# Kernel optimization log

Hardware: AMD Instinct MI355X
Metric: run time of the kernel (lower is better)

Reference implementation:

```python
import jax, jax.numpy as jnp
import numpy as np

N_NODES = 50000
N_EDGES = 600000
EMB = 128

def setup_inputs() -> dict:
    key = jax.random.key(0)
    ks = jax.random.split(key, 6)
    h = jax.random.normal(ks[0], (N_NODES, EMB), dtype=jnp.float32)
    edge_attr = jax.random.normal(ks[1], (N_EDGES, EMB), dtype=jnp.float32)
    src = jax.random.randint(ks[2], (N_EDGES,), 0, N_NODES, dtype=jnp.int32)
    dst = jax.random.randint(ks[3], (N_EDGES,), 0, N_NODES, dtype=jnp.int32)
    # MLP: Linear(emb, 2*emb) -> ReLU -> Linear(2*emb, emb)
    W1 = jax.random.normal(ks[4], (EMB, 2 * EMB), dtype=jnp.float32) * (1.0 / np.sqrt(EMB))
    b1 = jnp.zeros((2 * EMB,), dtype=jnp.float32)
    W2 = jax.random.normal(ks[5], (2 * EMB, EMB), dtype=jnp.float32) * (1.0 / np.sqrt(2 * EMB))
    b2 = jnp.zeros((EMB,), dtype=jnp.float32)
    eps = jnp.zeros((1,), dtype=jnp.float32)
    return {"h": h, "edge_attr": edge_attr, "src": src, "dst": dst,
            "W1": W1, "b1": b1, "W2": W2, "b2": b2, "eps": eps}

def reference(h, edge_attr, src, dst, W1, b1, W2, b2, eps):
    # message: m_e = h[src_e] + edge_attr_e   (edge_encoder is None)
    m = h[src] + edge_attr                              # [E, D]
    # reduce: sum messages per destination node
    aggr = jax.ops.segment_sum(m, dst, num_segments=N_NODES)  # [N, D]
    # out = (1 + eps) * h + MLP(aggr)
    hidden = jax.nn.relu(aggr @ W1 + b1)                # [N, 2D]
    mlp_out = hidden @ W2 + b2                          # [N, D]
    return (1.0 + eps) * h + mlp_out
```

## Files before the change

kernel.cpp:

```cpp
#include <hip/hip_runtime.h>
#include <hip/hip_bf16.h>

#define N_NODES 50000
#define N_EDGES 600000
#define D 128
#define H2 256
#define TN 16
#define MAXC 2048

__global__ __launch_bounds__(256) void hist_kernel(const int* __restrict__ dst,
                                                   int* __restrict__ counts) {
    unsigned int e = blockIdx.x * 256u + threadIdx.x;
    if (e < N_EDGES) atomicAdd(&counts[dst[e]], 1);
}

__global__ __launch_bounds__(256) void scan1_kernel(const int* __restrict__ counts,
                                                    int* __restrict__ scanned,
                                                    int* __restrict__ blocksums) {
    __shared__ int wsum[4];
    const int tid = threadIdx.x;
    const int lane = tid & 63;
    const int wv = tid >> 6;
    const int i = blockIdx.x * 256 + tid;
    const int cval = (i < N_NODES) ? counts[i] : 0;
    int x = cval;
    #pragma unroll
    for (int d = 1; d < 64; d <<= 1) {
        int t = __shfl_up(x, d, 64);
        if (lane >= d) x += t;
    }
    if (lane == 63) wsum[wv] = x;
    __syncthreads();
    if (tid == 0) {
        int s = 0;
        #pragma unroll
        for (int w = 0; w < 4; ++w) { s += wsum[w]; wsum[w] = s; }
    }
    __syncthreads();
    const int prefix = (wv > 0 ? wsum[wv - 1] : 0) + (x - cval);
    if (i < N_NODES) scanned[i] = prefix;
    if (tid == 0) blocksums[blockIdx.x] = wsum[3];
}

__global__ __launch_bounds__(256) void scan2_kernel(const int* __restrict__ blocksums,
                                                    int* __restrict__ blockbase, int nb) {
    __shared__ int wsum[4];
    const int tid = threadIdx.x;
    const int lane = tid & 63;
    const int wv = tid >> 6;
    const int cval = (tid < nb) ? blocksums[tid] : 0;
    int x = cval;
    #pragma unroll
    for (int d = 1; d < 64; d <<= 1) {
        int t = __shfl_up(x, d, 64);
        if (lane >= d) x += t;
    }
    if (lane == 63) wsum[wv] = x;
    __syncthreads();
    if (tid == 0) {
        int s = 0;
        #pragma unroll
        for (int w = 0; w < 4; ++w) { s += wsum[w]; wsum[w] = s; }
    }
    __syncthreads();
    if (tid < nb) blockbase[tid] = (wv > 0 ? wsum[wv - 1] : 0) + (x - cval);
}

__global__ __launch_bounds__(256) void scan3_kernel(const int* __restrict__ scanned,
                                                    const int* __restrict__ blockbase,
                                                    int* __restrict__ offsets,
                                                    int* __restrict__ cursor) {
    const int i = blockIdx.x * 256 + threadIdx.x;
    if (i < N_NODES) {
        const int v = scanned[i] + blockbase[blockIdx.x];
        offsets[i] = v;
        cursor[i] = v;
    }
    if (i == 0) offsets[N_NODES] = N_EDGES;
}

__global__ __launch_bounds__(256) void scatter_kernel(const int* __restrict__ src,
                                                      const int* __restrict__ dst,
                                                      int* __restrict__ cursor,
                                                      int2* __restrict__ perm2) {
    unsigned int e = blockIdx.x * 256u + threadIdx.x;
    if (e >= N_EDGES) return;
    const int d = dst[e];
    const int p = atomicAdd(&cursor[d], 1);
    perm2[p] = make_int2((int)e | ((d & (TN - 1)) << 20), src[e]);
}

__global__ __launch_bounds__(256) void fused_kernel(
    const float* __restrict__ h, const float* __restrict__ ea,
    const int* __restrict__ offsets, const int2* __restrict__ perm2,
    const float* __restrict__ W1, const float* __restrict__ b1,
    const float* __restrict__ W2, const float* __restrict__ b2,
    const float* __restrict__ eps, float* __restrict__ out)
{
    __shared__ float s_aggr[TN][D];
    __shared__ float s_hidden[TN][H2];
    int2* s_perm = (int2*)&s_hidden[0][0];

    const int tid = threadIdx.x;
    const int node0 = blockIdx.x * TN;

    for (int i = tid; i < TN * D / 4; i += 256)
        ((float4*)s_aggr)[i] = make_float4(0.f, 0.f, 0.f, 0.f);

    const int beg = offsets[node0];
    const int end = offsets[node0 + TN];
    const int grp = tid >> 5;
    const int c = (tid & 31) << 2;

    for (int cb = beg; cb < end; cb += MAXC) {
        const int cnt = min(end - cb, MAXC);
        __syncthreads();
        for (int i = tid; i < cnt; i += 256) s_perm[i] = perm2[cb + i];
        __syncthreads();
        const int per = (cnt + 7) >> 3;
        const int lo = grp * per;
        const int hi = min(lo + per, cnt);
        float4 acc = make_float4(0.f, 0.f, 0.f, 0.f);
        int tcur = -1;
        for (int j = lo; j < hi; ++j) {
            const int2 p = s_perm[j];
            const int t = p.x >> 20;
            const int e = p.x & 0xFFFFF;
            const float4 ev = *(const float4*)(ea + (size_t)e * D + c);
            const float4 hv = *(const float4*)(h + (size_t)p.y * D + c);
            if (t != tcur) {
                if (tcur >= 0) {
                    atomicAdd(&s_aggr[tcur][c + 0], acc.x);
                    atomicAdd(&s_aggr[tcur][c + 1], acc.y);
                    atomicAdd(&s_aggr[tcur][c + 2], acc.z);
                    atomicAdd(&s_aggr[tcur][c + 3], acc.w);
                }
                acc = make_float4(0.f, 0.f, 0.f, 0.f);
                tcur = t;
            }
            acc.x += ev.x + hv.x;
            acc.y += ev.y + hv.y;
            acc.z += ev.z + hv.z;
            acc.w += ev.w + hv.w;
        }
        if (tcur >= 0) {
            atomicAdd(&s_aggr[tcur][c + 0], acc.x);
            atomicAdd(&s_aggr[tcur][c + 1], acc.y);
            atomicAdd(&s_aggr[tcur][c + 2], acc.z);
            atomicAdd(&s_aggr[tcur][c + 3], acc.w);
        }
    }
    __syncthreads();

    {
        const int j0 = (tid & 63) << 2;
        const int tbase = (tid >> 6) << 2;
        float4 acc1[4];
        const float4 bv = *(const float4*)(b1 + j0);
        #pragma unroll
        for (int t = 0; t < 4; ++t) acc1[t] = bv;
        for (int k = 0; k < D; k += 4) {
            float4 w[4];
            #pragma unroll
            for (int q = 0; q < 4; ++q)
                w[q] = *(const float4*)(W1 + (size_t)(k + q) * H2 + j0);
            #pragma unroll
            for (int t = 0; t < 4; ++t) {
                const float4 a = *(const float4*)&s_aggr[tbase + t][k];
                acc1[t].x = fmaf(a.x, w[0].x, acc1[t].x);
                acc1[t].y = fmaf(a.x, w[0].y, acc1[t].y);
                acc1[t].z = fmaf(a.x, w[0].z, acc1[t].z);
                acc1[t].w = fmaf(a.x, w[0].w, acc1[t].w);
                acc1[t].x = fmaf(a.y, w[1].x, acc1[t].x);
                acc1[t].y = fmaf(a.y, w[1].y, acc1[t].y);
                acc1[t].z = fmaf(a.y, w[1].z, acc1[t].z);
                acc1[t].w = fmaf(a.y, w[1].w, acc1[t].w);
                acc1[t].x = fmaf(a.z, w[2].x, acc1[t].x);
                acc1[t].y = fmaf(a.z, w[2].y, acc1[t].y);
                acc1[t].z = fmaf(a.z, w[2].z, acc1[t].z);
                acc1[t].w = fmaf(a.z, w[2].w, acc1[t].w);
                acc1[t].x = fmaf(a.w, w[3].x, acc1[t].x);
                acc1[t].y = fmaf(a.w, w[3].y, acc1[t].y);
                acc1[t].z = fmaf(a.w, w[3].z, acc1[t].z);
                acc1[t].w = fmaf(a.w, w[3].w, acc1[t].w);
            }
        }
        __syncthreads();
        #pragma unroll
        for (int t = 0; t < 4; ++t) {
            float4 r;
            r.x = fmaxf(acc1[t].x, 0.f);
            r.y = fmaxf(acc1[t].y, 0.f);
            r.z = fmaxf(acc1[t].z, 0.f);
            r.w = fmaxf(acc1[t].w, 0.f);
            *(float4*)&s_hidden[tbase + t][j0] = r;
        }
    }
    __syncthreads();

    {
        const int i0 = (tid & 31) << 2;
        const int g = tid >> 5;
        float4 acc2[2];
        const float4 bv = *(const float4*)(b2 + i0);
        acc2[0] = bv; acc2[1] = bv;
        for (int k = 0; k < H2; k += 4) {
            float4 w[4];
            #pragma unroll
            for (int q = 0; q < 4; ++q)
                w[q] = *(const float4*)(W2 + (size_t)(k + q) * D + i0);
            #pragma unroll
            for (int u = 0; u < 2; ++u) {
                const float4 a = *(const float4*)&s_hidden[g + u * 8][k];
                acc2[u].x = fmaf(a.x, w[0].x, acc2[u].x);
                acc2[u].y = fmaf(a.x, w[0].y, acc2[u].y);
                acc2[u].z = fmaf(a.x, w[0].z, acc2[u].z);
                acc2[u].w = fmaf(a.x, w[0].w, acc2[u].w);
                acc2[u].x = fmaf(a.y, w[1].x, acc2[u].x);
                acc2[u].y = fmaf(a.y, w[1].y, acc2[u].y);
                acc2[u].z = fmaf(a.y, w[1].z, acc2[u].z);
                acc2[u].w = fmaf(a.y, w[1].w, acc2[u].w);
                acc2[u].x = fmaf(a.z, w[2].x, acc2[u].x);
                acc2[u].y = fmaf(a.z, w[2].y, acc2[u].y);
                acc2[u].z = fmaf(a.z, w[2].z, acc2[u].z);
                acc2[u].w = fmaf(a.z, w[2].w, acc2[u].w);
                acc2[u].x = fmaf(a.w, w[3].x, acc2[u].x);
                acc2[u].y = fmaf(a.w, w[3].y, acc2[u].y);
                acc2[u].z = fmaf(a.w, w[3].z, acc2[u].z);
                acc2[u].w = fmaf(a.w, w[3].w, acc2[u].w);
            }
        }
        const float ep = 1.0f + eps[0];
        #pragma unroll
        for (int u = 0; u < 2; ++u) {
            const int node = node0 + g + u * 8;
            const float4 hv = *(const float4*)(h + (size_t)node * D + i0);
            float4 o;
            o.x = fmaf(ep, hv.x, acc2[u].x);
            o.y = fmaf(ep, hv.y, acc2[u].y);
            o.z = fmaf(ep, hv.z, acc2[u].z);
            o.w = fmaf(ep, hv.w, acc2[u].w);
            *(float4*)(out + (size_t)node * D + i0) = o;
        }
    }
}

extern "C" void kernel_launch(void* const* d_in, const int* in_sizes, int n_in,
                              void* d_out, int out_size, void* d_ws, size_t ws_size,
                              hipStream_t stream) {
    const float* h   = (const float*)d_in[0];
    const float* ea  = (const float*)d_in[1];
    const int*   src = (const int*)d_in[2];
    const int*   dst = (const int*)d_in[3];
    const float* W1  = (const float*)d_in[4];
    const float* b1  = (const float*)d_in[5];
    const float* W2  = (const float*)d_in[6];
    const float* b2  = (const float*)d_in[7];
    const float* eps = (const float*)d_in[8];
    float* out = (float*)d_out;

    char* ws = (char*)d_ws;
    int*  counts    = (int*)ws;
    int*  scanned   = (int*)(ws + 256 * 1024);
    int*  offsets   = (int*)(ws + 512 * 1024);
    int*  cursor    = (int*)(ws + 768 * 1024);
    int*  blocksums = (int*)(ws + 1008 * 1024);
    int*  blockbase = (int*)(ws + 1012 * 1024);
    int2* perm2     = (int2*)(ws + 1024 * 1024);

    hipMemsetAsync(counts, 0, N_NODES * sizeof(int), stream);

    const int eblocks = (N_EDGES + 255) / 256;
    const int nblocks = (N_NODES + 255) / 256;

    hist_kernel<<<eblocks, 256, 0, stream>>>(dst, counts);
    scan1_kernel<<<nblocks, 256, 0, stream>>>(counts, scanned, blocksums);
    scan2_kernel<<<1, 256, 0, stream>>>(blocksums, blockbase, nblocks);
    scan3_kernel<<<nblocks, 256, 0, stream>>>(scanned, blockbase, offsets, cursor);
    scatter_kernel<<<eblocks, 256, 0, stream>>>(src, dst, cursor, perm2);
    fused_kernel<<<N_NODES / TN, 256, 0, stream>>>(
        h, ea, offsets, perm2, W1, b1, W2, b2, eps, out);
}
```

Before: 661.2 us.

## Merge CSR build into one cooperative kernel and unroll edge gather by four

Replaces the memset plus five CSR-construction kernels (histogram, three-stage scan, scatter) with a single cooperative kernel that separates phases with grid-wide syncs, removing per-launch overhead and gaps between launches. Separately, the edge-aggregation loop in the fused kernel now issues four edge_attr and h row loads before consuming them, to expose more memory-level parallelism. Risks: grid.sync costs and a 256x1024 grid that must be fully co-resident, plus extra register pressure from the unrolled loads.

```diff
diff --git a/kernel.cpp b/kernel.cpp
--- a/kernel.cpp
+++ b/kernel.cpp
@@ -1,5 +1,8 @@
 #include <hip/hip_runtime.h>
 #include <hip/hip_bf16.h>
+#include <hip/hip_cooperative_groups.h>
+
+namespace cg = cooperative_groups;
 
 #define N_NODES 50000
 #define N_EDGES 600000
@@ -8,86 +11,82 @@
 #define TN 16
 #define MAXC 2048
 
-__global__ __launch_bounds__(256) void hist_kernel(const int* __restrict__ dst,
-                                                   int* __restrict__ counts) {
-    unsigned int e = blockIdx.x * 256u + threadIdx.x;
-    if (e < N_EDGES) atomicAdd(&counts[dst[e]], 1);
-}
-
-__global__ __launch_bounds__(256) void scan1_kernel(const int* __restrict__ counts,
-                                                    int* __restrict__ scanned,
-                                                    int* __restrict__ blocksums) {
-    __shared__ int wsum[4];
+#define BUILD_BLOCKS 256
+#define BUILD_THREADS 1024
+#define NCHUNK ((N_NODES + 1023) / 1024)
+
+__global__ __launch_bounds__(BUILD_THREADS) void build_kernel(
+    const int* __restrict__ src, const int* __restrict__ dst,
+    int* __restrict__ counts, int* __restrict__ offsets,
+    int* __restrict__ cursor, int* __restrict__ blocksums,
+    int2* __restrict__ perm2)
+{
+    cg::grid_group grid = cg::this_grid();
+    __shared__ int wsum[16];
     const int tid = threadIdx.x;
+    const int bid = blockIdx.x;
+    const int gtid = bid * BUILD_THREADS + tid;
+    const int gsize = BUILD_BLOCKS * BUILD_THREADS;
     const int lane = tid & 63;
     const int wv = tid >> 6;
-    const int i = blockIdx.x * 256 + tid;
-    const int cval = (i < N_NODES) ? counts[i] : 0;
-    int x = cval;
-    #pragma unroll
-    for (int d = 1; d < 64; d <<= 1) {
-        int t = __shfl_up(x, d, 64);
-        if (lane >= d) x += t;
-    }
-    if (lane == 63) wsum[wv] = x;
-    __syncthreads();
-    if (tid == 0) {
-        int s = 0;
-        #pragma unroll
-        for (int w = 0; w < 4; ++w) { s += wsum[w]; wsum[w] = s; }
-    }
-    __syncthreads();
-    const int prefix = (wv > 0 ? wsum[wv - 1] : 0) + (x - cval);
-    if (i < N_NODES) scanned[i] = prefix;
-    if (tid == 0) blocksums[blockIdx.x] = wsum[3];
-}
-
-__global__ __launch_bounds__(256) void scan2_kernel(const int* __restrict__ blocksums,
-                                                    int* __restrict__ blockbase, int nb) {
-    __shared__ int wsum[4];
-    const int tid = threadIdx.x;
-    const int lane = tid & 63;
-    const int wv = tid >> 6;
-    const int cval = (tid < nb) ? blocksums[tid] : 0;
-    int x = cval;
-    #pragma unroll
-    for (int d = 1; d < 64; d <<= 1) {
-        int t = __shfl_up(x, d, 64);
-        if (lane >= d) x += t;
-    }
-    if (lane == 63) wsum[wv] = x;
-    __syncthreads();
-    if (tid == 0) {
-        int s = 0;
-        #pragma unroll
-        for (int w = 0; w < 4; ++w) { s += wsum[w]; wsum[w] = s; }
-    }
-    __syncthreads();
-    if (tid < nb) blockbase[tid] = (wv > 0 ? wsum[wv - 1] : 0) + (x - cval);
-}
-
-__global__ __launch_bounds__(256) void scan3_kernel(const int* __restrict__ scanned,
-                                                    const int* __restrict__ blockbase,
-                                                    int* __restrict__ offsets,
-                                                    int* __restrict__ cursor) {
-    const int i = blockIdx.x * 256 + threadIdx.x;
-    if (i < N_NODES) {
-        const int v = scanned[i] + blockbase[blockIdx.x];
-        offsets[i] = v;
-        cursor[i] = v;
-    }
-    if (i == 0) offsets[N_NODES] = N_EDGES;
-}
-
-__global__ __launch_bounds__(256) void scatter_kernel(const int* __restrict__ src,
-                                                      const int* __restrict__ dst,
-                                                      int* __restrict__ cursor,
-                                                      int2* __restrict__ perm2) {
-    unsigned int e = blockIdx.x * 256u + threadIdx.x;
-    if (e >= N_EDGES) return;
-    const int d = dst[e];
-    const int p = atomicAdd(&cursor[d], 1);
-    perm2[p] = make_int2((int)e | ((d & (TN - 1)) << 20), src[e]);
+
+    for (int i = gtid; i < N_NODES; i += gsize) counts[i] = 0;
+    grid.sync();
+
+    for (int e = gtid; e < N_EDGES; e += gsize) atomicAdd(&counts[dst[e]], 1);
+    grid.sync();
+
+    int myscan = 0;
+    if (bid < NCHUNK) {
+        const int i = bid * 1024 + tid;
+        const int myval = (i < N_NODES) ? counts[i] : 0;
+        int x = myval;
+        #pragma unroll
+        for (int d = 1; d < 64; d <<= 1) {
+            int t = __shfl_up(x, d, 64);
+            if (lane >= d) x += t;
+        }
+        if (lane == 63) wsum[wv] = x;
+        __syncthreads();
+        if (tid == 0) {
+            int s = 0;
+            #pragma unroll
+            for (int w = 0; w < 16; ++w) { s += wsum[w]; wsum[w] = s; }
+        }
+        __syncthreads();
+        myscan = (wv > 0 ? wsum[wv - 1] : 0) + (x - myval);
+        if (tid == 0) blocksums[bid] = wsum[15];
+    }
+    grid.sync();
+
+    if (bid == 0 && tid < 64) {
+        const int v = (tid < NCHUNK) ? blocksums[tid] : 0;
+        int x = v;
+        #pragma unroll
+        for (int d = 1; d < 64; d <<= 1) {
+            int t = __shfl_up(x, d, 64);
+            if (lane >= d) x += t;
+        }
+        if (tid < NCHUNK) blocksums[64 + tid] = x - v;
+    }
+    grid.sync();
+
+    if (bid < NCHUNK) {
+        const int i = bid * 1024 + tid;
+        if (i < N_NODES) {
+            const int v = myscan + blocksums[64 + bid];
+            offsets[i] = v;
+            cursor[i] = v;
+        }
+    }
+    if (gtid == 0) offsets[N_NODES] = N_EDGES;
+    grid.sync();
+
+    for (int e = gtid; e < N_EDGES; e += gsize) {
+        const int d = dst[e];
+        const int p = atomicAdd(&cursor[d], 1);
+        perm2[p] = make_int2(e | ((d & (TN - 1)) << 20), src[e]);
+    }
 }
 
 __global__ __launch_bounds__(256) void fused_kernel(
@@ -122,26 +121,38 @@
         const int hi = min(lo + per, cnt);
         float4 acc = make_float4(0.f, 0.f, 0.f, 0.f);
         int tcur = -1;
-        for (int j = lo; j < hi; ++j) {
-            const int2 p = s_perm[j];
-            const int t = p.x >> 20;
-            const int e = p.x & 0xFFFFF;
-            const float4 ev = *(const float4*)(ea + (size_t)e * D + c);
-            const float4 hv = *(const float4*)(h + (size_t)p.y * D + c);
-            if (t != tcur) {
-                if (tcur >= 0) {
-                    atomicAdd(&s_aggr[tcur][c + 0], acc.x);
-                    atomicAdd(&s_aggr[tcur][c + 1], acc.y);
-                    atomicAdd(&s_aggr[tcur][c + 2], acc.z);
-                    atomicAdd(&s_aggr[tcur][c + 3], acc.w);
+        for (int j = lo; j < hi; j += 4) {
+            const int nb = hi - j;
+            int2 p[4];
+            #pragma unroll
+            for (int u = 0; u < 4; ++u)
+                p[u] = s_perm[min(j + u, hi - 1)];
+            float4 ev[4], hv[4];
+            #pragma unroll
+            for (int u = 0; u < 4; ++u) {
+                ev[u] = *(const float4*)(ea + (size_t)(p[u].x & 0xFFFFF) * D + c);
+                hv[u] = *(const float4*)(h + (size_t)p[u].y * D + c);
+            }
+            #pragma unroll
+            for (int u = 0; u < 4; ++u) {
+                if (u < nb) {
+                    const int t = p[u].x >> 20;
+                    if (t != tcur) {
+                        if (tcur >= 0) {
+                            atomicAdd(&s_aggr[tcur][c + 0], acc.x);
+                            atomicAdd(&s_aggr[tcur][c + 1], acc.y);
+                            atomicAdd(&s_aggr[tcur][c + 2], acc.z);
+                            atomicAdd(&s_aggr[tcur][c + 3], acc.w);
+                        }
+                        acc = make_float4(0.f, 0.f, 0.f, 0.f);
+                        tcur = t;
+                    }
+                    acc.x += ev[u].x + hv[u].x;
+                    acc.y += ev[u].y + hv[u].y;
+                    acc.z += ev[u].z + hv[u].z;
+                    acc.w += ev[u].w + hv[u].w;
                 }
-                acc = make_float4(0.f, 0.f, 0.f, 0.f);
-                tcur = t;
-            }
-            acc.x += ev.x + hv.x;
-            acc.y += ev.y + hv.y;
-            acc.z += ev.z + hv.z;
-            acc.w += ev.w + hv.w;
+            }
         }
         if (tcur >= 0) {
             atomicAdd(&s_aggr[tcur][c + 0], acc.x);
@@ -261,23 +272,16 @@
 
     char* ws = (char*)d_ws;
     int*  counts    = (int*)ws;
-    int*  scanned   = (int*)(ws + 256 * 1024);
-    int*  offsets   = (int*)(ws + 512 * 1024);
-    int*  cursor    = (int*)(ws + 768 * 1024);
-    int*  blocksums = (int*)(ws + 1008 * 1024);
-    int*  blockbase = (int*)(ws + 1012 * 1024);
+    int*  offsets   = (int*)(ws + 256 * 1024);
+    int*  cursor    = (int*)(ws + 512 * 1024);
+    int*  blocksums = (int*)(ws + 768 * 1024);
     int2* perm2     = (int2*)(ws + 1024 * 1024);
 
-    hipMemsetAsync(counts, 0, N_NODES * sizeof(int), stream);
-
-    const int eblocks = (N_EDGES + 255) / 256;
-    const int nblocks = (N_NODES + 255) / 256;
-
-    hist_kernel<<<eblocks, 256, 0, stream>>>(dst, counts);
-    scan1_kernel<<<nblocks, 256, 0, stream>>>(counts, scanned, blocksums);
-    scan2_kernel<<<1, 256, 0, stream>>>(blocksums, blockbase, nblocks);
-    scan3_kernel<<<nblocks, 256, 0, stream>>>(scanned, blockbase, offsets, cursor);
-    scatter_kernel<<<eblocks, 256, 0, stream>>>(src, dst, cursor, perm2);
+    void* args[] = { (void*)&src, (void*)&dst, (void*)&counts, (void*)&offsets,
+                     (void*)&cursor, (void*)&blocksums, (void*)&perm2 };
+    hipLaunchCooperativeKernel((void*)build_kernel, dim3(BUILD_BLOCKS),
+                               dim3(BUILD_THREADS), args, 0, stream);
+
     fused_kernel<<<N_NODES / TN, 256, 0, stream>>>(
         h, ea, offsets, perm2, W1, b1, W2, b2, eps, out);
 }
```

New measurement: 789.4 us. 1.19x slower.
